# Optimization experiments

Measured on AMD Instinct MI355X. Metric: run time of the kernel, lower is better.

Reference implementation:

```python
import jax, jax.numpy as jnp
import numpy as np
import math

B, LQ, D = 4, 1024, 2048
H, G = 16, 4            # n_heads, n_groups
HD = D // H             # 128
GS = H // G             # group_size = 4
PAST = 1024
LK = PAST + LQ
NEG = jnp.float32(-1e30)


def _rope(x, cos, sin):
    # x: [B, L, nh, HD]; cos/sin: [1, L, 1, HD//2]; llama-style complex rotation
    x1 = x[..., 0::2]
    x2 = x[..., 1::2]
    r1 = x1 * cos - x2 * sin
    r2 = x1 * sin + x2 * cos
    return jnp.stack([r1, r2], axis=-1).reshape(x.shape)


def setup_inputs() -> dict:
    key = jax.random.key(0)
    ks = jax.random.split(key, 12)
    s = 0.02
    x = jax.random.normal(ks[0], (B, LQ, D), jnp.float32)
    past_k = jax.random.normal(ks[1], (B, G, PAST, HD), jnp.float32)
    past_v = jax.random.normal(ks[2], (B, G, PAST, HD), jnp.float32)
    rotary_freqs = jax.random.uniform(ks[3], (LQ, HD // 2), jnp.float32) * 6.283
    # causal mask with cache: query i may attend to key j if j <= PAST + i
    q_pos = PAST + jnp.arange(LQ)[:, None]
    k_pos = jnp.arange(LK)[None, :]
    mask = (k_pos <= q_pos)  # [LQ, LK] bool
    Wq = jax.random.normal(ks[4], (D, D), jnp.float32) * s
    bq = jnp.zeros((D,), jnp.float32)
    Wk = jax.random.normal(ks[5], (D, G * HD), jnp.float32) * s
    bk = jnp.zeros((G * HD,), jnp.float32)
    Wv = jax.random.normal(ks[6], (D, G * HD), jnp.float32) * s
    bv = jnp.zeros((G * HD,), jnp.float32)
    Wo = jax.random.normal(ks[7], (D, D), jnp.float32) * s
    bo = jnp.zeros((D,), jnp.float32)
    return {"x": x, "mask": mask, "rotary_freqs": rotary_freqs,
            "past_k": past_k, "past_v": past_v,
            "Wq": Wq, "bq": bq, "Wk": Wk, "bk": bk,
            "Wv": Wv, "bv": bv, "Wo": Wo, "bo": bo}


def reference(x, mask, rotary_freqs, past_k, past_v, Wq, bq, Wk, bk, Wv, bv, Wo, bo):
    # projections (torch Linear math with weights stored [in, out])
    q = (x @ Wq + bq).reshape(B, LQ, H, HD)      # break_heads: [B,L,H,HD]
    k = (x @ Wk + bk).reshape(B, LQ, G, HD)      # [B,L,G,HD]
    v = (x @ Wv + bv).reshape(B, LQ, G, HD).transpose(0, 2, 1, 3)  # [B,G,L,HD]
    # RoPE on q,k then move heads forward (matches q.transpose(2,1))
    cos = jnp.cos(rotary_freqs)[None, :, None, :]
    sin = jnp.sin(rotary_freqs)[None, :, None, :]
    q = _rope(q, cos, sin).transpose(0, 2, 1, 3)  # [B,H,LQ,HD]
    k = _rope(k, cos, sin).transpose(0, 2, 1, 3)  # [B,G,LQ,HD]
    # KV cache append
    k = jnp.concatenate([past_k, k], axis=2)      # [B,G,LK,HD]
    v = jnp.concatenate([past_v, v], axis=2)
    # grouped-query attention
    qg = q.reshape(B, G, GS, LQ, HD)
    scores = jnp.einsum('bgsqd,bgkd->bgsqk', qg, k) / math.sqrt(HD)
    scores = jnp.where(mask[None, None, None, :, :], scores, NEG)
    att = jax.nn.softmax(scores, axis=-1)
    out = jnp.einsum('bgsqk,bgkd->bgsqd', att, v).reshape(B, H, LQ, HD)
    out = out.transpose(0, 2, 1, 3).reshape(B, LQ, D)  # concatenate_heads
    return out @ Wo + bo
```

## Files before the change

kernel.cpp:

```cpp
#include <hip/hip_runtime.h>

#define B_   4
#define LQ_  1024
#define D_   2048
#define H_   16
#define G_   4
#define HD_  128
#define GS_  4
#define PAST_ 1024
#define LK_  2048
#define NQKV 3072

typedef __attribute__((ext_vector_type(8))) short short8;
typedef __attribute__((ext_vector_type(4))) float f32x4;

__device__ __forceinline__ ushort f2b(float f) {
    unsigned u = __builtin_bit_cast(unsigned, f);
    u += 0x7FFF + ((u >> 16) & 1);
    return (ushort)(u >> 16);
}
__device__ __forceinline__ float b2f(ushort h) {
    unsigned u = ((unsigned)h) << 16;
    return __builtin_bit_cast(float, u);
}

#define GLD_LDS16(gp, lp) \
    __builtin_amdgcn_global_load_lds((__attribute__((address_space(1))) void*)(gp), \
                                     (__attribute__((address_space(3))) void*)(lp), 16, 0, 0)

__global__ __launch_bounds__(256) void prep_misc(const float* __restrict__ x,
                                                 ushort* __restrict__ xb,
                                                 const float* __restrict__ pk,
                                                 ushort* __restrict__ kc,
                                                 const float* __restrict__ bq,
                                                 const float* __restrict__ bk,
                                                 const float* __restrict__ bv,
                                                 float* __restrict__ bias) {
    int blk = blockIdx.x;
    int tid = threadIdx.x;
    if (blk < 8192) {
        int i = blk * 256 + tid;
        float4 v = ((const float4*)x)[i];
        ushort4 o;
        o.x = f2b(v.x); o.y = f2b(v.y); o.z = f2b(v.z); o.w = f2b(v.w);
        ((ushort4*)xb)[i] = o;
    } else if (blk < 10240) {
        int i = (blk - 8192) * 256 + tid;
        float4 v = ((const float4*)pk)[i];
        int bg  = i >> 15;
        int rem = i & 32767;
        ushort4 o;
        o.x = f2b(v.x); o.y = f2b(v.y); o.z = f2b(v.z); o.w = f2b(v.w);
        ((ushort4*)kc)[(size_t)bg * 65536 + rem] = o;
    } else {
        int i = (blk - 10240) * 256 + tid;
        if (i < 2048) bias[i] = bq[i];
        else if (i < 2560) bias[i] = bk[i - 2048];
        else if (i < 3072) bias[i] = bv[i - 2560];
    }
}

__global__ __launch_bounds__(256) void wtrans_all(const float* __restrict__ Wq,
                                                  const float* __restrict__ Wk,
                                                  const float* __restrict__ Wv,
                                                  const float* __restrict__ Wo,
                                                  ushort* __restrict__ wt_qkv,
                                                  ushort* __restrict__ wt_o) {
    __shared__ float t[32][33];
    int blk = blockIdx.x;
    const float* in; ushort* out; int cols, bx, by;
    if (blk < 4096)      { in = Wq; out = wt_qkv;                        cols = 2048; bx = blk & 63; by = blk >> 6; }
    else if (blk < 5120) { int i = blk - 4096; in = Wk; out = wt_qkv + (size_t)2048 * 2048; cols = 512; bx = i & 15; by = i >> 4; }
    else if (blk < 6144) { int i = blk - 5120; in = Wv; out = wt_qkv + (size_t)2560 * 2048; cols = 512; bx = i & 15; by = i >> 4; }
    else                 { int i = blk - 6144; in = Wo; out = wt_o;      cols = 2048; bx = i & 63; by = i >> 6; }
    int c0 = bx * 32, r0 = by * 32;
    int tx = threadIdx.x, ty = threadIdx.y;
    #pragma unroll
    for (int i = 0; i < 32; i += 8)
        t[ty + i][tx] = in[(long)(r0 + ty + i) * cols + c0 + tx];
    __syncthreads();
    #pragma unroll
    for (int i = 0; i < 32; i += 8)
        out[(long)(c0 + ty + i) * 2048 + r0 + tx] = f2b(t[tx][ty + i]);
}

__global__ __launch_bounds__(256) void transpose_pack(const float* __restrict__ in,
                                                      ushort* __restrict__ out,
                                                      int rows_in, int cols_in,
                                                      long in_bstride, long out_bstride,
                                                      int out_rstride) {
    __shared__ float t[32][33];
    int bz = blockIdx.z;
    in  += (long)bz * in_bstride;
    out += (long)bz * out_bstride;
    int c0 = blockIdx.x * 32, r0 = blockIdx.y * 32;
    int tx = threadIdx.x, ty = threadIdx.y;
    #pragma unroll
    for (int i = 0; i < 32; i += 8) {
        int r = r0 + ty + i;
        if (r < rows_in && (c0 + tx) < cols_in)
            t[ty + i][tx] = in[(long)r * cols_in + c0 + tx];
    }
    __syncthreads();
    #pragma unroll
    for (int i = 0; i < 32; i += 8) {
        int c = c0 + ty + i, r = r0 + tx;
        if (c < cols_in && r < rows_in)
            out[(long)c * out_rstride + r] = f2b(t[tx][ty + i]);
    }
}

__global__ __launch_bounds__(256) void vtrans(const ushort* __restrict__ qkvb,
                                              ushort* __restrict__ vtc) {
    __shared__ ushort t[64][70];
    const int bg = blockIdx.z;
    const int b = bg >> 2, g = bg & 3;
    const int d0 = blockIdx.x * 64, q0 = blockIdx.y * 64;
    const int tx = threadIdx.x, ty = threadIdx.y;
    const ushort* src = qkvb + (size_t)(b * 1024 + q0) * NQKV + 2560 + g * 128 + d0;
    #pragma unroll
    for (int i = 0; i < 64; i += 4)
        t[ty + i][tx] = src[(size_t)(ty + i) * NQKV + tx];
    __syncthreads();
    ushort* dst = vtc + ((size_t)bg * 128 + d0) * LK_ + PAST_ + q0;
    #pragma unroll
    for (int i = 0; i < 64; i += 4)
        dst[(size_t)(ty + i) * LK_ + tx] = t[tx][ty + i];
}

template <bool BF16_OUT>
__global__ __launch_bounds__(512, 2) void gemm256(const ushort* __restrict__ Ap,
                                                  const ushort* __restrict__ Bp,
                                                  const float* __restrict__ bias,
                                                  void* __restrict__ Cout,
                                                  int M, int N, int K) {
    __shared__ ushort sh[65536];
    const int tid = threadIdx.x;
    const int w = tid >> 6, lane = tid & 63;
    const int quad = lane >> 4, l15 = lane & 15;
    const int wr = w >> 2, wc = w & 3;
    const int m0 = blockIdx.y * 256, n0 = blockIdx.x * 256;

    const int u0 = w * 64 + lane, u1 = (8 + w) * 64 + lane;
    const int r0_ = u0 >> 3, s0_ = u0 & 7;
    const int r1_ = u1 >> 3, s1_ = u1 & 7;
    const int sw0 = (s0_ ^ (r0_ & 7)) << 3, sw1 = (s1_ ^ (r1_ & 7)) << 3;
    const int srcA00 = (m0 + r0_) * K + sw0;
    const int srcA01 = (m0 + r1_) * K + sw1;
    const int srcA10 = (m0 + 128 + r0_) * K + sw0;
    const int srcA11 = (m0 + 128 + r1_) * K + sw1;
    const int srcB00 = (n0 + r0_) * K + sw0;
    const int srcB01 = (n0 + r1_) * K + sw1;
    const int srcB10 = (n0 + 128 + r0_) * K + sw0;
    const int srcB11 = (n0 + 128 + r1_) * K + sw1;

#define STAGE_A0(t, bufx) do { ushort* d_ = sh + (bufx) * 32768 + w * 512; \
    GLD_LDS16(Ap + (size_t)(srcA00 + (t) * 64), d_); \
    GLD_LDS16(Ap + (size_t)(srcA01 + (t) * 64), d_ + 4096); } while (0)
#define STAGE_A1(t, bufx) do { ushort* d_ = sh + (bufx) * 32768 + 8192 + w * 512; \
    GLD_LDS16(Ap + (size_t)(srcA10 + (t) * 64), d_); \
    GLD_LDS16(Ap + (size_t)(srcA11 + (t) * 64), d_ + 4096); } while (0)
#define STAGE_B0(t, bufx) do { ushort* d_ = sh + (bufx) * 32768 + 16384 + w * 512; \
    GLD_LDS16(Bp + (size_t)(srcB00 + (t) * 64), d_); \
    GLD_LDS16(Bp + (size_t)(srcB01 + (t) * 64), d_ + 4096); } while (0)
#define STAGE_B1(t, bufx) do { ushort* d_ = sh + (bufx) * 32768 + 16384 + 8192 + w * 512; \
    GLD_LDS16(Bp + (size_t)(srcB10 + (t) * 64), d_); \
    GLD_LDS16(Bp + (size_t)(srcB11 + (t) * 64), d_ + 4096); } while (0)

#define READ_A(QR) \
    _Pragma("unroll") for (int fi = 0; fi < 4; ++fi) \
    _Pragma("unroll") for (int ks = 0; ks < 2; ++ks) \
        a[fi * 2 + ks] = *(const short8*)(Ab + (wr * 128 + (QR) * 64 + fi * 16 + l15) * 64 + \
                                          (((ks * 4 + quad) ^ (l15 & 7)) << 3));
#define READ_B(QC, BREG) \
    _Pragma("unroll") for (int fj = 0; fj < 2; ++fj) \
    _Pragma("unroll") for (int ks = 0; ks < 2; ++ks) \
        BREG[fj * 2 + ks] = *(const short8*)(Bb + (wc * 64 + (QC) * 32 + fj * 16 + l15) * 64 + \
                                             (((ks * 4 + quad) ^ (l15 & 7)) << 3));
#define MFMA_Q(QR, QC, BREG) \
    _Pragma("unroll") for (int ks = 0; ks < 2; ++ks) \
    _Pragma("unroll") for (int fj = 0; fj < 2; ++fj) \
    _Pragma("unroll") for (int fi = 0; fi < 4; ++fi) \
        acc[(QR) * 4 + fi][(QC) * 2 + fj] = __builtin_amdgcn_mfma_f32_16x16x32_bf16( \
            a[fi * 2 + ks], BREG[fj * 2 + ks], acc[(QR) * 4 + fi][(QC) * 2 + fj], 0, 0, 0);

#define PH_MID() do { asm volatile("" ::: "memory"); __builtin_amdgcn_s_barrier(); \
    asm volatile("s_waitcnt lgkmcnt(0)" ::: "memory"); __builtin_amdgcn_sched_barrier(0); \
    __builtin_amdgcn_s_setprio(1); } while (0)
#define PH_END() do { __builtin_amdgcn_s_setprio(0); asm volatile("" ::: "memory"); \
    __builtin_amdgcn_s_barrier(); asm volatile("" ::: "memory"); } while (0)

    f32x4 acc[8][4];
    #pragma unroll
    for (int i = 0; i < 8; ++i)
        #pragma unroll
        for (int j = 0; j < 4; ++j)
            #pragma unroll
            for (int r = 0; r < 4; ++r) acc[i][j][r] = 0.f;

    const int KT = K >> 6;

    STAGE_A0(0, 0); STAGE_A1(0, 0); STAGE_B0(0, 0); STAGE_B1(0, 0);
    STAGE_B0(1, 1); STAGE_B1(1, 1);
    asm volatile("s_waitcnt vmcnt(4)" ::: "memory");
    asm volatile("" ::: "memory");
    __builtin_amdgcn_s_barrier();
    asm volatile("" ::: "memory");

    short8 a[8], b0[4], b1[4];
    for (int t = 0; t < KT; ++t) {
        const int buf = t & 1;
        const ushort* Ab = sh + buf * 32768;
        const ushort* Bb = Ab + 16384;

        READ_A(0)
        READ_B(0, b0)
        if (t + 1 < KT) STAGE_A0(t + 1, buf ^ 1);
        PH_MID();
        MFMA_Q(0, 0, b0)
        PH_END();

        READ_B(1, b1)
        if (t + 1 < KT) STAGE_A1(t + 1, buf ^ 1);
        PH_MID();
        MFMA_Q(0, 1, b1)
        PH_END();

        READ_A(1)
        if (t + 2 < KT) STAGE_B0(t + 2, buf);
        PH_MID();
        MFMA_Q(1, 0, b0)
        PH_END();

        if (t + 2 < KT) {
            STAGE_B1(t + 2, buf);
            asm volatile("s_waitcnt vmcnt(4)" ::: "memory");
        } else {
            asm volatile("s_waitcnt vmcnt(0)" ::: "memory");
        }
        PH_MID();
        MFMA_Q(1, 1, b1)
        PH_END();
    }

    #pragma unroll
    for (int fi = 0; fi < 8; ++fi)
        #pragma unroll
        for (int fj = 0; fj < 4; ++fj)
            #pragma unroll
            for (int r = 0; r < 4; ++r) {
                int row = m0 + wr * 128 + fi * 16 + quad * 4 + r;
                int col = n0 + wc * 64 + fj * 16 + l15;
                float v = acc[fi][fj][r] + bias[col];
                if (BF16_OUT) ((ushort*)Cout)[(size_t)row * N + col] = f2b(v);
                else          ((float*)Cout)[(size_t)row * N + col] = v;
            }
#undef STAGE_A0
#undef STAGE_A1
#undef STAGE_B0
#undef STAGE_B1
#undef READ_A
#undef READ_B
#undef MFMA_Q
#undef PH_MID
#undef PH_END
}

template <bool BF16_OUT>
__global__ __launch_bounds__(512, 2) void gemm_128x256(const ushort* __restrict__ Ap,
                                                       const ushort* __restrict__ Bp,
                                                       const float* __restrict__ bias,
                                                       void* __restrict__ Cout,
                                                       int M, int N, int K) {
    __shared__ ushort sh[49152];
    const int tid = threadIdx.x;
    const int w = tid >> 6, lane = tid & 63;
    const int quad = lane >> 4, l15 = lane & 15;
    const int wr = w >> 2, wc = w & 3;
    const int m0 = blockIdx.y * 128, n0 = blockIdx.x * 256;

    const int u0 = w * 64 + lane, u1 = (8 + w) * 64 + lane;
    const int r0_ = u0 >> 3, s0_ = u0 & 7;
    const int r1_ = u1 >> 3, s1_ = u1 & 7;
    const int sw0 = (s0_ ^ (r0_ & 7)) << 3, sw1 = (s1_ ^ (r1_ & 7)) << 3;
    const int srcA0  = (m0 + r0_) * K + sw0;
    const int srcA1  = (m0 + 64 + r0_) * K + sw0;
    const int srcB00 = (n0 + r0_) * K + sw0;
    const int srcB01 = (n0 + r1_) * K + sw1;
    const int srcB10 = (n0 + 128 + r0_) * K + sw0;
    const int srcB11 = (n0 + 128 + r1_) * K + sw1;

#define STG_A0(t, bufx) do { ushort* d_ = sh + (bufx) * 24576 + w * 512; \
    GLD_LDS16(Ap + (size_t)(srcA0 + (t) * 64), d_); } while (0)
#define STG_A1(t, bufx) do { ushort* d_ = sh + (bufx) * 24576 + 4096 + w * 512; \
    GLD_LDS16(Ap + (size_t)(srcA1 + (t) * 64), d_); } while (0)
#define STG_B0(t, bufx) do { ushort* d_ = sh + (bufx) * 24576 + 8192 + w * 512; \
    GLD_LDS16(Bp + (size_t)(srcB00 + (t) * 64), d_); \
    GLD_LDS16(Bp + (size_t)(srcB01 + (t) * 64), d_ + 4096); } while (0)
#define STG_B1(t, bufx) do { ushort* d_ = sh + (bufx) * 24576 + 16384 + w * 512; \
    GLD_LDS16(Bp + (size_t)(srcB10 + (t) * 64), d_); \
    GLD_LDS16(Bp + (size_t)(srcB11 + (t) * 64), d_ + 4096); } while (0)

#define RD_A(QR) \
    _Pragma("unroll") for (int fi = 0; fi < 2; ++fi) \
    _Pragma("unroll") for (int ks = 0; ks < 2; ++ks) \
        a[fi * 2 + ks] = *(const short8*)(Ab + (wr * 64 + (QR) * 32 + fi * 16 + l15) * 64 + \
                                          (((ks * 4 + quad) ^ (l15 & 7)) << 3));
#define RD_B(QC, BREG) \
    _Pragma("unroll") for (int fj = 0; fj < 2; ++fj) \
    _Pragma("unroll") for (int ks = 0; ks < 2; ++ks) \
        BREG[fj * 2 + ks] = *(const short8*)(Bb + (wc * 64 + (QC) * 32 + fj * 16 + l15) * 64 + \
                                             (((ks * 4 + quad) ^ (l15 & 7)) << 3));
#define MM_Q(QR, QC, BREG) \
    _Pragma("unroll") for (int ks = 0; ks < 2; ++ks) \
    _Pragma("unroll") for (int fj = 0; fj < 2; ++fj) \
    _Pragma("unroll") for (int fi = 0; fi < 2; ++fi) \
        acc[(QR) * 2 + fi][(QC) * 2 + fj] = __builtin_amdgcn_mfma_f32_16x16x32_bf16( \
            a[fi * 2 + ks], BREG[fj * 2 + ks], acc[(QR) * 2 + fi][(QC) * 2 + fj], 0, 0, 0);

#define PH_MID() do { asm volatile("" ::: "memory"); __builtin_amdgcn_s_barrier(); \
    asm volatile("s_waitcnt lgkmcnt(0)" ::: "memory"); __builtin_amdgcn_sched_barrier(0); \
    __builtin_amdgcn_s_setprio(1); } while (0)
#define PH_END() do { __builtin_amdgcn_s_setprio(0); asm volatile("" ::: "memory"); \
    __builtin_amdgcn_s_barrier(); asm volatile("" ::: "memory"); } while (0)

    f32x4 acc[4][4];
    #pragma unroll
    for (int i = 0; i < 4; ++i)
        #pragma unroll
        for (int j = 0; j < 4; ++j)
            #pragma unroll
            for (int r = 0; r < 4; ++r) acc[i][j][r] = 0.f;

    const int KT = K >> 6;

    STG_A0(0, 0); STG_A1(0, 0); STG_B0(0, 0); STG_B1(0, 0);
    STG_B0(1, 1); STG_B1(1, 1);
    asm volatile("s_waitcnt vmcnt(4)" ::: "memory");
    asm volatile("" ::: "memory");
    __builtin_amdgcn_s_barrier();
    asm volatile("" ::: "memory");

    short8 a[4], b0[4], b1[4];
    for (int t = 0; t < KT; ++t) {
        const int buf = t & 1;
        const ushort* Ab = sh + buf * 24576;
        const ushort* Bb = Ab + 8192;

        RD_A(0)
        RD_B(0, b0)
        if (t + 1 < KT) STG_A0(t + 1, buf ^ 1);
        PH_MID();
        MM_Q(0, 0, b0)
        PH_END();

        RD_B(1, b1)
        if (t + 1 < KT) STG_A1(t + 1, buf ^ 1);
        PH_MID();
        MM_Q(0, 1, b1)
        PH_END();

        RD_A(1)
        if (t + 2 < KT) STG_B0(t + 2, buf);
        PH_MID();
        MM_Q(1, 0, b0)
        PH_END();

        if (t + 2 < KT) {
            STG_B1(t + 2, buf);
            asm volatile("s_waitcnt vmcnt(4)" ::: "memory");
        } else {
            asm volatile("s_waitcnt vmcnt(0)" ::: "memory");
        }
        PH_MID();
        MM_Q(1, 1, b1)
        PH_END();
    }

    #pragma unroll
    for (int fi = 0; fi < 4; ++fi)
        #pragma unroll
        for (int fj = 0; fj < 4; ++fj)
            #pragma unroll
            for (int r = 0; r < 4; ++r) {
                int row = m0 + wr * 64 + fi * 16 + quad * 4 + r;
                int col = n0 + wc * 64 + fj * 16 + l15;
                float v = acc[fi][fj][r] + bias[col];
                if (BF16_OUT) ((ushort*)Cout)[(size_t)row * N + col] = f2b(v);
                else          ((float*)Cout)[(size_t)row * N + col] = v;
            }
#undef STG_A0
#undef STG_A1
#undef STG_B0
#undef STG_B1
#undef RD_A
#undef RD_B
#undef MM_Q
#undef PH_MID
#undef PH_END
}

__global__ __launch_bounds__(256) void rope_pack(const ushort* __restrict__ qkvb,
                                                 const float* __restrict__ rf,
                                                 ushort* __restrict__ qb,
                                                 ushort* __restrict__ kc) {
    const float SC = 0.08838834764831845f;
    int row = blockIdx.x;
    int b = row >> 10, qi = row & 1023;
    int tid = threadIdx.x;
    const ushort* src = qkvb + (size_t)row * NQKV;

    for (int p = tid; p < 1024; p += 256) {
        int h = p >> 6, i = p & 63;
        float fr = rf[qi * 64 + i];
        float s, c; __sincosf(fr, &s, &c);
        uint pr = *(const uint*)(src + h * 128 + 2 * i);
        float x1 = b2f((ushort)(pr & 0xffff));
        float x2 = b2f((ushort)(pr >> 16));
        float r1 = (x1 * c - x2 * s) * SC;
        float r2 = (x1 * s + x2 * c) * SC;
        size_t o = (((size_t)(b * H_ + h)) * LQ_ + qi) * HD_ + 2 * i;
        *(uint*)(qb + o) = (uint)f2b(r1) | ((uint)f2b(r2) << 16);
    }
    {
        int g = tid >> 6, i = tid & 63;
        float fr = rf[qi * 64 + i];
        float s, c; __sincosf(fr, &s, &c);
        uint pr = *(const uint*)(src + 2048 + g * 128 + 2 * i);
        float x1 = b2f((ushort)(pr & 0xffff));
        float x2 = b2f((ushort)(pr >> 16));
        float r1 = x1 * c - x2 * s;
        float r2 = x1 * s + x2 * c;
        size_t o = (((size_t)(b * G_ + g)) * LK_ + PAST_ + qi) * HD_ + 2 * i;
        *(uint*)(kc + o) = (uint)f2b(r1) | ((uint)f2b(r2) << 16);
    }
}

__global__ __launch_bounds__(256, 2) void attn_kernel(const ushort* __restrict__ qb,
                                                      const ushort* __restrict__ kc,
                                                      const ushort* __restrict__ vtc,
                                                      ushort* __restrict__ attn_a) {
    __shared__ ushort kt[2][64 * 128];
    __shared__ ushort vtt[2][128 * 64];
    __shared__ ushort pt[128 * 64];

    const int tid = threadIdx.x;
    const int wave = tid >> 6, lane = tid & 63;
    const int quad = lane >> 4, l15 = lane & 15;
    const int qh = wave >> 1;
    const int jw = wave & 1;
    const int tile = (blockIdx.y < 32) ? blockIdx.x : (7 - (int)blockIdx.x);
    const int q0 = tile << 7;
    const int bh = blockIdx.y;
    const int b = bh >> 4, h = bh & 15, g = h >> 2;
    const ushort* kcb = kc + ((size_t)(b * G_ + g)) * LK_ * HD_;
    const ushort* vcb = vtc + ((size_t)(b * G_ + g)) * HD_ * LK_;

    int ksrc[4], vsrc[4];
    #pragma unroll
    for (int i = 0; i < 4; ++i) {
        int u = (wave * 4 + i) * 64 + lane;
        int key = u >> 4, cs = u & 15;
        ksrc[i] = key * HD_ + ((cs ^ (key & 15)) << 3);
        int d = u >> 3, c2 = u & 7;
        vsrc[i] = d * LK_ + ((c2 ^ (d & 7)) << 3);
    }

    short8 qf[4][4];
    #pragma unroll
    for (int qfr = 0; qfr < 4; ++qfr) {
        int qrow = q0 + qh * 64 + qfr * 16 + l15;
        const ushort* qp = qb + (((size_t)(b * H_ + h)) * LQ_ + qrow) * HD_ + quad * 8;
        #pragma unroll
        for (int kk = 0; kk < 4; ++kk) qf[qfr][kk] = *(const short8*)(qp + kk * 32);
    }

    f32x4 o[4][4];
    #pragma unroll
    for (int qfr = 0; qfr < 4; ++qfr)
        #pragma unroll
        for (int f = 0; f < 4; ++f)
            #pragma unroll
            for (int r = 0; r < 4; ++r) o[qfr][f][r] = 0.f;
    float lstq[4];
    #pragma unroll
    for (int qfr = 0; qfr < 4; ++qfr) lstq[qfr] = 0.f;

    const int nsteps = (PAST_ + q0 + 128) >> 6;

    #pragma unroll
    for (int i = 0; i < 4; ++i) {
        int ci = wave * 4 + i;
        GLD_LDS16(kcb + ksrc[i], kt[0] + ci * 512);
        GLD_LDS16(vcb + vsrc[i], vtt[0] + ci * 512);
    }

    for (int it = 0; it < nsteps; ++it) {
        const int k0 = it << 6;
        const int cur = it & 1, nxt = cur ^ 1;
        __syncthreads();
        if (it + 1 < nsteps) {
            const int k1 = k0 + 64;
            #pragma unroll
            for (int i = 0; i < 4; ++i) {
                int ci = wave * 4 + i;
                GLD_LDS16(kcb + (size_t)k1 * HD_ + ksrc[i], kt[nxt] + ci * 512);
                GLD_LDS16(vcb + k1 + vsrc[i], vtt[nxt] + ci * 512);
            }
        }

        f32x4 z[4][2];
        #pragma unroll
        for (int qfr = 0; qfr < 4; ++qfr)
            #pragma unroll
            for (int kf = 0; kf < 2; ++kf)
                #pragma unroll
                for (int r = 0; r < 4; ++r) z[qfr][kf][r] = 0.f;
        __builtin_amdgcn_s_setprio(1);
        #pragma unroll
        for (int kk = 0; kk < 4; ++kk) {
            #pragma unroll
            for (int kf = 0; kf < 2; ++kf) {
                int key = jw * 32 + kf * 16 + l15;
                const short8 bk = *(const short8*)(kt[cur] + key * 128 + (((kk * 4 + quad) ^ l15) << 3));
                #pragma unroll
                for (int qfr = 0; qfr < 4; ++qfr)
                    z[qfr][kf] = __builtin_amdgcn_mfma_f32_16x16x32_bf16(bk, qf[qfr][kk], z[qfr][kf], 0, 0, 0);
            }
        }
        __builtin_amdgcn_s_setprio(0);

        const bool mask_step = (it >= nsteps - 2);
        #pragma unroll
        for (int qfr = 0; qfr < 4; ++qfr) {
            const int row = qh * 64 + qfr * 16 + l15;
            #pragma unroll
            for (int kf = 0; kf < 2; ++kf) {
                float pv0[4];
                #pragma unroll
                for (int r = 0; r < 4; ++r) {
                    float pv_ = __expf(z[qfr][kf][r]);
                    if (mask_step) {
                        int keyg = k0 + jw * 32 + kf * 16 + quad * 4 + r;
                        if (keyg > PAST_ + q0 + row) pv_ = 0.f;
                    }
                    lstq[qfr] += pv_;
                    pv0[r] = pv_;
                }
                uint2 val;
                val.x = (uint)f2b(pv0[0]) | ((uint)f2b(pv0[1]) << 16);
                val.y = (uint)f2b(pv0[2]) | ((uint)f2b(pv0[3]) << 16);
                int unit = jw * 4 + kf * 2 + (quad >> 1);
                int swz = ((unit ^ (row & 7)) << 3) + ((quad & 1) << 2);
                *(uint2*)(pt + row * 64 + swz) = val;
            }
        }

        asm volatile("s_waitcnt lgkmcnt(0)" ::: "memory");
        __builtin_amdgcn_s_barrier();
        __builtin_amdgcn_sched_barrier(0);

        __builtin_amdgcn_s_setprio(1);
        #pragma unroll
        for (int j2 = 0; j2 < 2; ++j2) {
            short8 pa[4];
            #pragma unroll
            for (int qfr = 0; qfr < 4; ++qfr) {
                int prow = qh * 64 + qfr * 16 + l15;
                pa[qfr] = *(const short8*)(pt + prow * 64 + (((j2 * 4 + quad) ^ (prow & 7)) << 3));
            }
            #pragma unroll
            for (int f = 0; f < 4; ++f) {
                int d = jw * 64 + f * 16 + l15;
                const short8 bv = *(const short8*)(vtt[cur] + d * 64 + (((j2 * 4 + quad) ^ (l15 & 7)) << 3));
                #pragma unroll
                for (int qfr = 0; qfr < 4; ++qfr)
                    o[qfr][f] = __builtin_amdgcn_mfma_f32_16x16x32_bf16(pa[qfr], bv, o[qfr][f], 0, 0, 0);
            }
        }
        __builtin_amdgcn_s_setprio(0);
    }

    float rq[4];
    #pragma unroll
    for (int qfr = 0; qfr < 4; ++qfr) {
        float rs = lstq[qfr];
        rs += __shfl_xor(rs, 16);
        rs += __shfl_xor(rs, 32);
        rq[qfr] = rs;
    }
    __syncthreads();
    float* scr = (float*)pt;
    #pragma unroll
    for (int qfr = 0; qfr < 4; ++qfr)
        scr[wave * 256 + qfr * 64 + lane] = rq[qfr];
    __syncthreads();
    #pragma unroll
    for (int qfr = 0; qfr < 4; ++qfr) {
        float tot = rq[qfr] + scr[(wave ^ 1) * 256 + qfr * 64 + lane];
        float linv[4];
        #pragma unroll
        for (int r = 0; r < 4; ++r)
            linv[r] = 1.0f / __shfl(tot, quad * 4 + r, 16);
        #pragma unroll
        for (int f = 0; f < 4; ++f)
            #pragma unroll
            for (int r = 0; r < 4; ++r) {
                int q = q0 + qh * 64 + qfr * 16 + quad * 4 + r;
                int d = jw * 64 + f * 16 + l15;
                attn_a[((size_t)(b * LQ_ + q)) * D_ + h * HD_ + d] = f2b(o[qfr][f][r] * linv[r]);
            }
    }
}


extern "C" void kernel_launch(void* const* d_in, const int* in_sizes, int n_in,
                              void* d_out, int out_size, void* d_ws, size_t ws_size,
                              hipStream_t stream) {
    const float* x  = (const float*)d_in[0];
    const float* rf = (const float*)d_in[2];
    const float* pk = (const float*)d_in[3];
    const float* pv = (const float*)d_in[4];
    const float* Wq = (const float*)d_in[5];
    const float* bq = (const float*)d_in[6];
    const float* Wk = (const float*)d_in[7];
    const float* bk = (const float*)d_in[8];
    const float* Wv = (const float*)d_in[9];
    const float* bv = (const float*)d_in[10];
    const float* Wo = (const float*)d_in[11];
    const float* bo = (const float*)d_in[12];
    float* out = (float*)d_out;

    char* p = (char*)d_ws;
    auto take = [&](size_t n) { void* r = p; p += (n + 255) & ~(size_t)255; return r; };
    ushort* xb       = (ushort*)take((size_t)4096 * 2048 * 2);
    ushort* wt_qkv   = (ushort*)take((size_t)3072 * 2048 * 2);
    ushort* wt_o     = (ushort*)take((size_t)2048 * 2048 * 2);
    float*  bias_qkv = (float*) take((size_t)3072 * 4);
    ushort* qkvb     = (ushort*)take((size_t)4096 * 3072 * 2);
    ushort* qb       = (ushort*)take((size_t)B_ * H_ * LQ_ * HD_ * 2);
    ushort* kcache   = (ushort*)take((size_t)B_ * G_ * LK_ * HD_ * 2);
    ushort* vtc      = (ushort*)take((size_t)B_ * G_ * HD_ * LK_ * 2);
    ushort* attn_a   = (ushort*)take((size_t)4096 * 2048 * 2);

    prep_misc<<<10252, 256, 0, stream>>>(x, xb, pk, kcache, bq, bk, bv, bias_qkv);
    wtrans_all<<<10240, dim3(32, 8), 0, stream>>>(Wq, Wk, Wv, Wo, wt_qkv, wt_o);
    transpose_pack<<<dim3(4, 32, 16), dim3(32, 8), 0, stream>>>(pv, vtc, 1024, 128,
                                                                (long)1024 * 128, (long)128 * 2048, 2048);

    gemm256<true><<<dim3(12, 16), 512, 0, stream>>>(xb, wt_qkv, bias_qkv, qkvb, 4096, 3072, 2048);
    rope_pack<<<4096, 256, 0, stream>>>(qkvb, rf, qb, kcache);
    vtrans<<<dim3(2, 16, 16), dim3(64, 4), 0, stream>>>(qkvb, vtc);
    attn_kernel<<<dim3(8, 64), 256, 0, stream>>>(qb, kcache, vtc, attn_a);
    gemm_128x256<false><<<dim3(8, 32), 512, 0, stream>>>(attn_a, wt_o, bo, out, 4096, 2048, 2048);
}
```

Before: 354.3 us.

## Merge prep kernels, fuse rope with V transpose, use exp2 and packed bf16 converts

Folds the three preprocessing kernels (x/past_k conversion, weight transposes, past_v transpose) into one launch, and merges RoPE packing with the V transpose into a second single launch, cutting five launches down to two. The Q scale now includes log2(e) so the attention softmax can use exp2f instead of __expf. Manual round-to-nearest bf16 packing is replaced by the hardware v_cvt_pk_bf16_f32 instruction. The merged kernels carry branch divergence and a shared LDS allocation sized for the largest branch, which may affect occupancy.

```diff
diff --git a/kernel.cpp b/kernel.cpp
--- a/kernel.cpp
+++ b/kernel.cpp
@@ -23,109 +23,83 @@
     unsigned u = ((unsigned)h) << 16;
     return __builtin_bit_cast(float, u);
 }
+__device__ __forceinline__ uint pk2(float lo, float hi) {
+    uint r;
+    asm("v_cvt_pk_bf16_f32 %0, %1, %2" : "=v"(r) : "v"(lo), "v"(hi));
+    return r;
+}
 
 #define GLD_LDS16(gp, lp) \
     __builtin_amdgcn_global_load_lds((__attribute__((address_space(1))) void*)(gp), \
                                      (__attribute__((address_space(3))) void*)(lp), 16, 0, 0)
 
-__global__ __launch_bounds__(256) void prep_misc(const float* __restrict__ x,
-                                                 ushort* __restrict__ xb,
-                                                 const float* __restrict__ pk,
-                                                 ushort* __restrict__ kc,
-                                                 const float* __restrict__ bq,
-                                                 const float* __restrict__ bk,
-                                                 const float* __restrict__ bv,
-                                                 float* __restrict__ bias) {
-    int blk = blockIdx.x;
-    int tid = threadIdx.x;
+__global__ __launch_bounds__(256) void prep_all(const float* __restrict__ x,
+                                                ushort* __restrict__ xb,
+                                                const float* __restrict__ pk,
+                                                ushort* __restrict__ kc,
+                                                const float* __restrict__ bq,
+                                                const float* __restrict__ bk,
+                                                const float* __restrict__ bv,
+                                                float* __restrict__ bias,
+                                                const float* __restrict__ Wq,
+                                                const float* __restrict__ Wk,
+                                                const float* __restrict__ Wv,
+                                                const float* __restrict__ Wo,
+                                                ushort* __restrict__ wt_qkv,
+                                                ushort* __restrict__ wt_o,
+                                                const float* __restrict__ pv,
+                                                ushort* __restrict__ vtc) {
+    __shared__ float t[32][33];
+    const int blk = blockIdx.x;
+    const int tid = threadIdx.x;
     if (blk < 8192) {
         int i = blk * 256 + tid;
         float4 v = ((const float4*)x)[i];
-        ushort4 o;
-        o.x = f2b(v.x); o.y = f2b(v.y); o.z = f2b(v.z); o.w = f2b(v.w);
-        ((ushort4*)xb)[i] = o;
+        uint2 o; o.x = pk2(v.x, v.y); o.y = pk2(v.z, v.w);
+        ((uint2*)xb)[i] = o;
     } else if (blk < 10240) {
         int i = (blk - 8192) * 256 + tid;
         float4 v = ((const float4*)pk)[i];
         int bg  = i >> 15;
         int rem = i & 32767;
-        ushort4 o;
-        o.x = f2b(v.x); o.y = f2b(v.y); o.z = f2b(v.z); o.w = f2b(v.w);
-        ((ushort4*)kc)[(size_t)bg * 65536 + rem] = o;
-    } else {
+        uint2 o; o.x = pk2(v.x, v.y); o.y = pk2(v.z, v.w);
+        ((uint2*)kc)[(size_t)bg * 65536 + rem] = o;
+    } else if (blk < 10252) {
         int i = (blk - 10240) * 256 + tid;
         if (i < 2048) bias[i] = bq[i];
         else if (i < 2560) bias[i] = bk[i - 2048];
         else if (i < 3072) bias[i] = bv[i - 2560];
-    }
-}
-
-__global__ __launch_bounds__(256) void wtrans_all(const float* __restrict__ Wq,
-                                                  const float* __restrict__ Wk,
-                                                  const float* __restrict__ Wv,
-                                                  const float* __restrict__ Wo,
-                                                  ushort* __restrict__ wt_qkv,
-                                                  ushort* __restrict__ wt_o) {
-    __shared__ float t[32][33];
-    int blk = blockIdx.x;
-    const float* in; ushort* out; int cols, bx, by;
-    if (blk < 4096)      { in = Wq; out = wt_qkv;                        cols = 2048; bx = blk & 63; by = blk >> 6; }
-    else if (blk < 5120) { int i = blk - 4096; in = Wk; out = wt_qkv + (size_t)2048 * 2048; cols = 512; bx = i & 15; by = i >> 4; }
-    else if (blk < 6144) { int i = blk - 5120; in = Wv; out = wt_qkv + (size_t)2560 * 2048; cols = 512; bx = i & 15; by = i >> 4; }
-    else                 { int i = blk - 6144; in = Wo; out = wt_o;      cols = 2048; bx = i & 63; by = i >> 6; }
-    int c0 = bx * 32, r0 = by * 32;
-    int tx = threadIdx.x, ty = threadIdx.y;
-    #pragma unroll
-    for (int i = 0; i < 32; i += 8)
-        t[ty + i][tx] = in[(long)(r0 + ty + i) * cols + c0 + tx];
-    __syncthreads();
-    #pragma unroll
-    for (int i = 0; i < 32; i += 8)
-        out[(long)(c0 + ty + i) * 2048 + r0 + tx] = f2b(t[tx][ty + i]);
-}
-
-__global__ __launch_bounds__(256) void transpose_pack(const float* __restrict__ in,
-                                                      ushort* __restrict__ out,
-                                                      int rows_in, int cols_in,
-                                                      long in_bstride, long out_bstride,
-                                                      int out_rstride) {
-    __shared__ float t[32][33];
-    int bz = blockIdx.z;
-    in  += (long)bz * in_bstride;
-    out += (long)bz * out_bstride;
-    int c0 = blockIdx.x * 32, r0 = blockIdx.y * 32;
-    int tx = threadIdx.x, ty = threadIdx.y;
-    #pragma unroll
-    for (int i = 0; i < 32; i += 8) {
-        int r = r0 + ty + i;
-        if (r < rows_in && (c0 + tx) < cols_in)
-            t[ty + i][tx] = in[(long)r * cols_in + c0 + tx];
-    }
-    __syncthreads();
-    #pragma unroll
-    for (int i = 0; i < 32; i += 8) {
-        int c = c0 + ty + i, r = r0 + tx;
-        if (c < cols_in && r < rows_in)
-            out[(long)c * out_rstride + r] = f2b(t[tx][ty + i]);
-    }
-}
-
-__global__ __launch_bounds__(256) void vtrans(const ushort* __restrict__ qkvb,
-                                              ushort* __restrict__ vtc) {
-    __shared__ ushort t[64][70];
-    const int bg = blockIdx.z;
-    const int b = bg >> 2, g = bg & 3;
-    const int d0 = blockIdx.x * 64, q0 = blockIdx.y * 64;
-    const int tx = threadIdx.x, ty = threadIdx.y;
-    const ushort* src = qkvb + (size_t)(b * 1024 + q0) * NQKV + 2560 + g * 128 + d0;
-    #pragma unroll
-    for (int i = 0; i < 64; i += 4)
-        t[ty + i][tx] = src[(size_t)(ty + i) * NQKV + tx];
-    __syncthreads();
-    ushort* dst = vtc + ((size_t)bg * 128 + d0) * LK_ + PAST_ + q0;
-    #pragma unroll
-    for (int i = 0; i < 64; i += 4)
-        dst[(size_t)(ty + i) * LK_ + tx] = t[tx][ty + i];
+    } else if (blk < 20492) {
+        int wblk = blk - 10252;
+        const float* in; ushort* out; int cols, bx, by;
+        if (wblk < 4096)      { in = Wq; out = wt_qkv;                               cols = 2048; bx = wblk & 63; by = wblk >> 6; }
+        else if (wblk < 5120) { int i = wblk - 4096; in = Wk; out = wt_qkv + (size_t)2048 * 2048; cols = 512; bx = i & 15; by = i >> 4; }
+        else if (wblk < 6144) { int i = wblk - 5120; in = Wv; out = wt_qkv + (size_t)2560 * 2048; cols = 512; bx = i & 15; by = i >> 4; }
+        else                  { int i = wblk - 6144; in = Wo; out = wt_o;            cols = 2048; bx = i & 63; by = i >> 6; }
+        int c0 = bx * 32, r0 = by * 32;
+        int tx = tid & 31, ty = tid >> 5;
+        #pragma unroll
+        for (int i = 0; i < 32; i += 8)
+            t[ty + i][tx] = in[(long)(r0 + ty + i) * cols + c0 + tx];
+        __syncthreads();
+        #pragma unroll
+        for (int i = 0; i < 32; i += 8)
+            out[(long)(c0 + ty + i) * 2048 + r0 + tx] = f2b(t[tx][ty + i]);
+    } else {
+        int pblk = blk - 20492;
+        int bx = pblk & 3, by = (pblk >> 2) & 31, bz = pblk >> 7;
+        const float* in = pv + (long)bz * 1024 * 128;
+        ushort* out = vtc + (long)bz * 128 * 2048;
+        int c0 = bx * 32, r0 = by * 32;
+        int tx = tid & 31, ty = tid >> 5;
+        #pragma unroll
+        for (int i = 0; i < 32; i += 8)
+            t[ty + i][tx] = in[(long)(r0 + ty + i) * 128 + c0 + tx];
+        __syncthreads();
+        #pragma unroll
+        for (int i = 0; i < 32; i += 8)
+            out[(long)(c0 + ty + i) * 2048 + r0 + tx] = f2b(t[tx][ty + i]);
+    }
 }
 
 template <bool BF16_OUT>
@@ -400,39 +374,53 @@
 #undef PH_END
 }
 
-__global__ __launch_bounds__(256) void rope_pack(const ushort* __restrict__ qkvb,
-                                                 const float* __restrict__ rf,
-                                                 ushort* __restrict__ qb,
-                                                 ushort* __restrict__ kc) {
-    const float SC = 0.08838834764831845f;
-    int row = blockIdx.x;
-    int b = row >> 10, qi = row & 1023;
-    int tid = threadIdx.x;
-    const ushort* src = qkvb + (size_t)row * NQKV;
-
-    for (int p = tid; p < 1024; p += 256) {
-        int h = p >> 6, i = p & 63;
-        float fr = rf[qi * 64 + i];
-        float s, c; __sincosf(fr, &s, &c);
-        uint pr = *(const uint*)(src + h * 128 + 2 * i);
-        float x1 = b2f((ushort)(pr & 0xffff));
-        float x2 = b2f((ushort)(pr >> 16));
-        float r1 = (x1 * c - x2 * s) * SC;
-        float r2 = (x1 * s + x2 * c) * SC;
-        size_t o = (((size_t)(b * H_ + h)) * LQ_ + qi) * HD_ + 2 * i;
-        *(uint*)(qb + o) = (uint)f2b(r1) | ((uint)f2b(r2) << 16);
-    }
-    {
-        int g = tid >> 6, i = tid & 63;
-        float fr = rf[qi * 64 + i];
-        float s, c; __sincosf(fr, &s, &c);
-        uint pr = *(const uint*)(src + 2048 + g * 128 + 2 * i);
-        float x1 = b2f((ushort)(pr & 0xffff));
-        float x2 = b2f((ushort)(pr >> 16));
-        float r1 = x1 * c - x2 * s;
-        float r2 = x1 * s + x2 * c;
-        size_t o = (((size_t)(b * G_ + g)) * LK_ + PAST_ + qi) * HD_ + 2 * i;
-        *(uint*)(kc + o) = (uint)f2b(r1) | ((uint)f2b(r2) << 16);
+__global__ __launch_bounds__(256) void rope_vtrans(const ushort* __restrict__ qkvb,
+                                                   const float* __restrict__ rf,
+                                                   ushort* __restrict__ qb,
+                                                   ushort* __restrict__ kc,
+                                                   ushort* __restrict__ vtc) {
+    __shared__ ushort t[64][70];
+    const int blk = blockIdx.x;
+    const int tid = threadIdx.x;
+    if (blk < 4096) {
+        const float SC2 = 0.12751743f;
+        int b = blk >> 10, qi = blk & 1023;
+        const ushort* src = qkvb + (size_t)blk * NQKV;
+        for (int p = tid; p < 1024; p += 256) {
+            int h = p >> 6, i = p & 63;
+            float fr = rf[qi * 64 + i];
+            float s, c; __sincosf(fr, &s, &c);
+            uint pr = *(const uint*)(src + h * 128 + 2 * i);
+            float x1 = b2f((ushort)(pr & 0xffff));
+            float x2 = b2f((ushort)(pr >> 16));
+            size_t o = (((size_t)(b * H_ + h)) * LQ_ + qi) * HD_ + 2 * i;
+            *(uint*)(qb + o) = pk2((x1 * c - x2 * s) * SC2, (x1 * s + x2 * c) * SC2);
+        }
+        {
+            int g = tid >> 6, i = tid & 63;
+            float fr = rf[qi * 64 + i];
+            float s, c; __sincosf(fr, &s, &c);
+            uint pr = *(const uint*)(src + 2048 + g * 128 + 2 * i);
+            float x1 = b2f((ushort)(pr & 0xffff));
+            float x2 = b2f((ushort)(pr >> 16));
+            size_t o = (((size_t)(b * G_ + g)) * LK_ + PAST_ + qi) * HD_ + 2 * i;
+            *(uint*)(kc + o) = pk2(x1 * c - x2 * s, x1 * s + x2 * c);
+        }
+    } else {
+        int i0 = blk - 4096;
+        int bx = i0 & 1, by = (i0 >> 1) & 15, bz = i0 >> 5;
+        int b = bz >> 2, g = bz & 3;
+        int d0 = bx * 64, q0v = by * 64;
+        int tx = tid & 63, ty = tid >> 6;
+        const ushort* src = qkvb + (size_t)(b * 1024 + q0v) * NQKV + 2560 + g * 128 + d0;
+        #pragma unroll
+        for (int i = 0; i < 64; i += 4)
+            t[ty + i][tx] = src[(size_t)(ty + i) * NQKV + tx];
+        __syncthreads();
+        ushort* dst = vtc + ((size_t)bz * 128 + d0) * LK_ + PAST_ + q0v;
+        #pragma unroll
+        for (int i = 0; i < 64; i += 4)
+            dst[(size_t)(ty + i) * LK_ + tx] = t[tx][ty + i];
     }
 }
 
@@ -539,7 +527,7 @@
                 float pv0[4];
                 #pragma unroll
                 for (int r = 0; r < 4; ++r) {
-                    float pv_ = __expf(z[qfr][kf][r]);
+                    float pv_ = exp2f(z[qfr][kf][r]);
                     if (mask_step) {
                         int keyg = k0 + jw * 32 + kf * 16 + quad * 4 + r;
                         if (keyg > PAST_ + q0 + row) pv_ = 0.f;
@@ -548,8 +536,8 @@
                     pv0[r] = pv_;
                 }
                 uint2 val;
-                val.x = (uint)f2b(pv0[0]) | ((uint)f2b(pv0[1]) << 16);
-                val.y = (uint)f2b(pv0[2]) | ((uint)f2b(pv0[3]) << 16);
+                val.x = pk2(pv0[0], pv0[1]);
+                val.y = pk2(pv0[2], pv0[3]);
                 int unit = jw * 4 + kf * 2 + (quad >> 1);
                 int swz = ((unit ^ (row & 7)) << 3) + ((quad & 1) << 2);
                 *(uint2*)(pt + row * 64 + swz) = val;
@@ -643,14 +631,10 @@
     ushort* vtc      = (ushort*)take((size_t)B_ * G_ * HD_ * LK_ * 2);
     ushort* attn_a   = (ushort*)take((size_t)4096 * 2048 * 2);
 
-    prep_misc<<<10252, 256, 0, stream>>>(x, xb, pk, kcache, bq, bk, bv, bias_qkv);
-    wtrans_all<<<10240, dim3(32, 8), 0, stream>>>(Wq, Wk, Wv, Wo, wt_qkv, wt_o);
-    transpose_pack<<<dim3(4, 32, 16), dim3(32, 8), 0, stream>>>(pv, vtc, 1024, 128,
-                                                                (long)1024 * 128, (long)128 * 2048, 2048);
-
+    prep_all<<<22540, 256, 0, stream>>>(x, xb, pk, kcache, bq, bk, bv, bias_qkv,
+                                        Wq, Wk, Wv, Wo, wt_qkv, wt_o, pv, vtc);
     gemm256<true><<<dim3(12, 16), 512, 0, stream>>>(xb, wt_qkv, bias_qkv, qkvb, 4096, 3072, 2048);
-    rope_pack<<<4096, 256, 0, stream>>>(qkvb, rf, qb, kcache);
-    vtrans<<<dim3(2, 16, 16), dim3(64, 4), 0, stream>>>(qkvb, vtc);
+    rope_vtrans<<<4608, 256, 0, stream>>>(qkvb, rf, qb, kcache, vtc);
     attn_kernel<<<dim3(8, 64), 256, 0, stream>>>(qb, kcache, vtc, attn_a);
     gemm_128x256<false><<<dim3(8, 32), 512, 0, stream>>>(attn_a, wt_o, bo, out, 4096, 2048, 2048);
 }
```

New measurement: 351.2 us. Within noise of the previous version (-0.9%).
